# Kernel tuning notes

Measured on AMD Instinct MI355X. Metric: run time of the kernel, lower is better.

Reference implementation:

```python
import jax, jax.numpy as jnp
import numpy as np

NUM_USERS = 50000
NUM_ITEMS = 50000
N_NODES = NUM_USERS + NUM_ITEMS
NNZ = 3200000
EMB_DIM = 64
N_LAYERS = 3
BATCH = 16384


def setup_inputs() -> dict:
    key = jax.random.key(0)
    ks = jax.random.split(key, 7)
    user_emb = 0.1 * jax.random.normal(ks[0], (NUM_USERS, EMB_DIM), dtype=jnp.float32)
    item_emb = 0.1 * jax.random.normal(ks[1], (NUM_ITEMS, EMB_DIM), dtype=jnp.float32)
    edge_val = jax.random.uniform(ks[2], (NNZ,), dtype=jnp.float32)
    edge_src = jax.random.randint(ks[3], (NNZ,), 0, N_NODES, dtype=jnp.int32)
    edge_dst = jax.random.randint(ks[4], (NNZ,), 0, N_NODES, dtype=jnp.int32)
    users = jax.random.randint(ks[5], (BATCH,), 0, NUM_USERS, dtype=jnp.int32)
    items = jax.random.randint(ks[6], (BATCH,), 0, NUM_ITEMS, dtype=jnp.int32)
    return {"user_emb": user_emb, "item_emb": item_emb, "edge_val": edge_val,
            "edge_src": edge_src, "edge_dst": edge_dst, "users": users, "items": items}


def _computer(user_emb, item_emb, edge_val, edge_src, edge_dst):
    # LightGCN propagation: all_emb <- A @ all_emb, mean over layer outputs (incl. layer 0)
    all_emb = jnp.concatenate([user_emb, item_emb], axis=0)  # [N, D]
    acc = all_emb
    for _ in range(N_LAYERS):
        msg = edge_val[:, None] * all_emb[edge_src]          # [nnz, D]
        all_emb = jax.ops.segment_sum(msg, edge_dst, num_segments=N_NODES)
        acc = acc + all_emb
    light_out = acc / jnp.float32(N_LAYERS + 1)
    return light_out[:NUM_USERS], light_out[NUM_USERS:]


def reference(user_emb, item_emb, edge_val, edge_src, edge_dst, users, items):
    all_users, all_items = _computer(user_emb, item_emb, edge_val, edge_src, edge_dst)
    users_emb = all_users[users]                              # [B, D]
    items_emb = all_items[items]                              # [B, D]
    gamma = jnp.sum(users_emb * items_emb, axis=1)            # [B]
    return gamma
```

## Files before the change

kernel.cpp:

```cpp
#include <hip/hip_runtime.h>

#define NUM_USERS 50000
#define NUM_ITEMS 50000
#define N_NODES   100000
#define NNZ       3200000
#define EMB_DIM   64
#define N_LAYERS  3
#define BATCH     16384

#define NBUCK 512
#define ABITS 8
#define NODES_PER_BUCK 256
#define TILE_EDGES 8192
#define NBUCK_USED ((N_NODES + NODES_PER_BUCK - 1) / NODES_PER_BUCK)
#define CAP 9216

typedef unsigned long long ull;
typedef float v2f __attribute__((ext_vector_type(2)));

__device__ inline unsigned bf16pair(float a, float b) {
    unsigned ua = __float_as_uint(a), ub = __float_as_uint(b);
    unsigned r0 = (ua + 0x7fffu + ((ua >> 16) & 1u)) >> 16;
    unsigned r1 = (ub + 0x7fffu + ((ub >> 16) & 1u)) >> 16;
    return r0 | (r1 << 16);
}
__device__ inline float blo(unsigned u) { return __uint_as_float(u << 16); }
__device__ inline float bhi(unsigned u) { return __uint_as_float(u & 0xffff0000u); }

__device__ inline void pkfma(v2f& d, v2f a, v2f b) {
    asm("v_pk_fma_f32 %0, %1, %2, %0" : "+v"(d) : "v"(a), "v"(b));
}
__device__ inline void pkadd(v2f& d, v2f a) {
    asm("v_pk_add_f32 %0, %1, %0" : "+v"(d) : "v"(a));
}

__device__ inline void accP(v2f& sA, v2f& sB, v2f& sC, v2f& sD, uint4 g, unsigned r) {
    float w = (float)(r >> 17);
    v2f w2 = {w, w};
    v2f e0 = {blo(g.x), bhi(g.x)};
    v2f e1 = {blo(g.y), bhi(g.y)};
    v2f e2 = {blo(g.z), bhi(g.z)};
    v2f e3 = {blo(g.w), bhi(g.w)};
    pkfma(sA, e0, w2);
    pkfma(sB, e1, w2);
    pkfma(sC, e2, w2);
    pkfma(sD, e3, w2);
}

__device__ inline uint4 gath(const unsigned char* __restrict__ base, unsigned r, unsigned dOff) {
    unsigned off = ((r & 0x1FFFFu) << 7) + dOff;
    return *(const uint4*)(base + off);
}

__device__ inline uint4 predload4(const unsigned* __restrict__ ep, int j, int b4, int cnt) {
    int i = j + b4;
    uint4 R = *(const uint4*)(ep + i);
    if (i + 1 > cnt) R.x = 0u;
    if (i + 2 > cnt) R.y = 0u;
    if (i + 3 > cnt) R.z = 0u;
    if (i + 4 > cnt) R.w = 0u;
    return R;
}

__device__ inline void wred(v2f& s) {
    v2f t;
    t.x = __shfl_xor(s.x, 8, 64);  t.y = __shfl_xor(s.y, 8, 64);  pkadd(s, t);
    t.x = __shfl_xor(s.x, 16, 64); t.y = __shfl_xor(s.y, 16, 64); pkadd(s, t);
    t.x = __shfl_xor(s.x, 32, 64); t.y = __shfl_xor(s.y, 32, 64); pkadd(s, t);
}

__global__ void init_emb_kernel(const float* __restrict__ ue,
                                const float* __restrict__ ie,
                                unsigned* __restrict__ E0,
                                int* __restrict__ bucketCursor,
                                unsigned char* __restrict__ flags,
                                const int* __restrict__ users,
                                const int* __restrict__ items) {
    int idx = blockIdx.x * blockDim.x + threadIdx.x;
    if (blockIdx.x == 0 && threadIdx.x < 256) {
        bucketCursor[threadIdx.x]       = threadIdx.x * CAP;
        bucketCursor[threadIdx.x + 256] = (threadIdx.x + 256) * CAP;
    }
    if (idx < BATCH) {
        flags[users[idx]] = 1;
    } else if (idx < 2 * BATCH) {
        flags[NUM_USERS + items[idx - BATCH]] = 1;
    }
    const int total = N_NODES * (EMB_DIM / 4);
    if (idx >= total) return;
    const int uoff = NUM_USERS * (EMB_DIM / 4);
    float4 v;
    if (idx < uoff) v = ((const float4*)ue)[idx];
    else            v = ((const float4*)ie)[idx - uoff];
    uint2 h;
    h.x = bf16pair(v.x, v.y);
    h.y = bf16pair(v.z, v.w);
    ((uint2*)E0)[idx] = h;
}

__global__ void partA_kernel(const float* __restrict__ ev,
                             const int*  __restrict__ es,
                             const int*  __restrict__ ed,
                             int* __restrict__ bucketCursor,
                             ull* __restrict__ tmp) {
    __shared__ int hist[NBUCK];
    __shared__ int base[NBUCK];
    __shared__ int cnt2[NBUCK];
    int tid = threadIdx.x;
    int e0 = blockIdx.x * TILE_EDGES;

    int      mySrc[8], myDst[8];
    unsigned myQ[8];

    for (int i = tid; i < NBUCK; i += 1024) hist[i] = 0;
    __syncthreads();

    #pragma unroll
    for (int k = 0; k < 8; ++k) {
        int e = e0 + k * 1024 + tid;
        if (e < NNZ) {
            mySrc[k] = es[e];
            myDst[k] = ed[e];
            myQ[k]   = (unsigned)fminf(ev[e] * 32768.f + 0.5f, 32767.f);
            atomicAdd(&hist[((unsigned)myDst[k]) >> ABITS], 1);
        } else {
            myDst[k] = -1;
        }
    }
    __syncthreads();

    for (int i = tid; i < NBUCK; i += 1024) {
        int c = hist[i];
        base[i] = c ? atomicAdd(&bucketCursor[i], c) : 0;
        cnt2[i] = 0;
    }
    __syncthreads();

    #pragma unroll
    for (int k = 0; k < 8; ++k) {
        int dst = myDst[k];
        if (dst < 0) continue;
        int b = ((unsigned)dst) >> ABITS;
        int pos = base[b] + atomicAdd(&cnt2[b], 1);
        if (pos < (b + 1) * CAP) {
            ull rec = (ull)(unsigned)(mySrc[k] | ((dst & (NODES_PER_BUCK - 1)) << 17))
                    | ((ull)myQ[k] << 25);
            tmp[pos] = rec;
        }
    }
}

__global__ void partB_kernel(const ull* __restrict__ tmp,
                             const int* __restrict__ bucketCursor,
                             int* __restrict__ rowStart,
                             int* __restrict__ deg,
                             unsigned* __restrict__ sorted) {
    __shared__ int cnt[NODES_PER_BUCK];
    __shared__ int sc[NODES_PER_BUCK];
    __shared__ int cur[NODES_PER_BUCK];
    int b = blockIdx.x;
    int tid = threadIdx.x;
    int nodeLo = b << ABITS;
    int startE = b * CAP;
    int endE   = bucketCursor[b];

    if (tid < NODES_PER_BUCK) cnt[tid] = 0;
    __syncthreads();

    ull myRec[9];
    int nRec = 0;
    #pragma unroll
    for (int k = 0; k < 9; ++k) {
        int i = startE + k * 1024 + tid;
        if (i < endE) {
            myRec[k] = tmp[i];
            nRec = k + 1;
            atomicAdd(&cnt[(int)((myRec[k] >> 17) & (NODES_PER_BUCK - 1))], 1);
        }
    }
    __syncthreads();

    if (tid < NODES_PER_BUCK) sc[tid] = (cnt[tid] + 3) & ~3;
    __syncthreads();
    for (int o = 1; o < NODES_PER_BUCK; o <<= 1) {
        int add = 0;
        if (tid < NODES_PER_BUCK && tid >= o) add = sc[tid - o];
        __syncthreads();
        if (tid < NODES_PER_BUCK) sc[tid] += add;
        __syncthreads();
    }
    if (tid < NODES_PER_BUCK) {
        int node = nodeLo + tid;
        int pc = (cnt[tid] + 3) & ~3;
        int rs = startE + sc[tid] - pc;
        cur[tid] = rs;
        if (node < N_NODES) {
            rowStart[node] = rs;
            deg[node] = cnt[tid];
        }
    }
    __syncthreads();

    for (int k = 0; k < nRec; ++k) {
        ull rec = myRec[k];
        int dl = (int)((rec >> 17) & (NODES_PER_BUCK - 1));
        unsigned o = (unsigned)(rec & 0x1FFFFULL) | ((unsigned)((rec >> 25) & 0x7FFF) << 17);
        int pos = atomicAdd(&cur[dl], 1);
        if (pos < startE + CAP) sorted[pos] = o;
    }
}

__global__ void __launch_bounds__(256, 4)
pull_kernel(const unsigned char* __restrict__ A16,
            uint4* __restrict__ B16,
            const unsigned* __restrict__ sorted,
            const int* __restrict__ rowStart,
            const int* __restrict__ deg,
            const unsigned char* __restrict__ flags,
            int gate) {
    int wid = __builtin_amdgcn_readfirstlane((blockIdx.x << 2) + (threadIdx.x >> 6));
    int n0 = wid << 1;
    if (n0 >= N_NODES) return;
    int lane = threadIdx.x & 63;
    int eg = lane >> 3;
    int b4 = eg << 2;
    unsigned dOff = (unsigned)(lane & 7) << 4;

    bool a0 = true, a1 = true;
    if (gate) {
        a0 = flags[n0] == 1;
        a1 = flags[n0 + 1] == 1;
        if (!(a0 || a1)) return;
    }
    int c0 = a0 ? deg[n0] : 0;
    int c1 = a1 ? deg[n0 + 1] : 0;
    const unsigned* ep0 = sorted + rowStart[n0];
    const unsigned* ep1 = sorted + rowStart[n0 + 1];

    bool u0a = c0 > 0,  u0b = c0 > 32;
    bool u1a = c1 > 0,  u1b = c1 > 32;

    uint4 R0a, R1a, R0b, R1b;
    if (u0a) R0a = predload4(ep0, 0,  b4, c0);
    if (u1a) R1a = predload4(ep1, 0,  b4, c1);
    if (u0b) R0b = predload4(ep0, 32, b4, c0);
    if (u1b) R1b = predload4(ep1, 32, b4, c1);

    v2f s0A = {0.f,0.f}, s0B = {0.f,0.f}, s0C = {0.f,0.f}, s0D = {0.f,0.f};
    v2f s1A = {0.f,0.f}, s1B = {0.f,0.f}, s1C = {0.f,0.f}, s1D = {0.f,0.f};

    uint4 G0a0, G0a1, G0a2, G0a3;
    uint4 G1a0, G1a1, G1a2, G1a3;
    uint4 G0b0, G0b1, G0b2, G0b3;
    uint4 G1b0, G1b1, G1b2, G1b3;
    if (u0a) {
        G0a0 = gath(A16, R0a.x, dOff); G0a1 = gath(A16, R0a.y, dOff);
        G0a2 = gath(A16, R0a.z, dOff); G0a3 = gath(A16, R0a.w, dOff);
    }
    if (u1a) {
        G1a0 = gath(A16, R1a.x, dOff); G1a1 = gath(A16, R1a.y, dOff);
        G1a2 = gath(A16, R1a.z, dOff); G1a3 = gath(A16, R1a.w, dOff);
    }
    if (u0b) {
        G0b0 = gath(A16, R0b.x, dOff); G0b1 = gath(A16, R0b.y, dOff);
        G0b2 = gath(A16, R0b.z, dOff); G0b3 = gath(A16, R0b.w, dOff);
    }

    if (u0a) {
        accP(s0A, s0B, s0C, s0D, G0a0, R0a.x);
        accP(s0A, s0B, s0C, s0D, G0a1, R0a.y);
        accP(s0A, s0B, s0C, s0D, G0a2, R0a.z);
        accP(s0A, s0B, s0C, s0D, G0a3, R0a.w);
    }
    if (u1b) {
        G1b0 = gath(A16, R1b.x, dOff); G1b1 = gath(A16, R1b.y, dOff);
        G1b2 = gath(A16, R1b.z, dOff); G1b3 = gath(A16, R1b.w, dOff);
    }
    if (u0b) {
        accP(s0A, s0B, s0C, s0D, G0b0, R0b.x);
        accP(s0A, s0B, s0C, s0D, G0b1, R0b.y);
        accP(s0A, s0B, s0C, s0D, G0b2, R0b.z);
        accP(s0A, s0B, s0C, s0D, G0b3, R0b.w);
    }
    if (u1a) {
        accP(s1A, s1B, s1C, s1D, G1a0, R1a.x);
        accP(s1A, s1B, s1C, s1D, G1a1, R1a.y);
        accP(s1A, s1B, s1C, s1D, G1a2, R1a.z);
        accP(s1A, s1B, s1C, s1D, G1a3, R1a.w);
    }
    if (u1b) {
        accP(s1A, s1B, s1C, s1D, G1b0, R1b.x);
        accP(s1A, s1B, s1C, s1D, G1b1, R1b.y);
        accP(s1A, s1B, s1C, s1D, G1b2, R1b.z);
        accP(s1A, s1B, s1C, s1D, G1b3, R1b.w);
    }

    if (__builtin_expect((c0 > 64) || (c1 > 64), 0)) {
        for (int j = 64; j < c0; j += 16) {
            int i0 = j + eg, i1 = j + 8 + eg;
            unsigned r0 = (i0 < c0) ? ep0[i0] : 0u;
            unsigned r1 = (i1 < c0) ? ep0[i1] : 0u;
            uint4 g0 = gath(A16, r0, dOff);
            uint4 g1 = gath(A16, r1, dOff);
            accP(s0A, s0B, s0C, s0D, g0, r0);
            accP(s0A, s0B, s0C, s0D, g1, r1);
        }
        for (int j = 64; j < c1; j += 16) {
            int i0 = j + eg, i1 = j + 8 + eg;
            unsigned r0 = (i0 < c1) ? ep1[i0] : 0u;
            unsigned r1 = (i1 < c1) ? ep1[i1] : 0u;
            uint4 g0 = gath(A16, r0, dOff);
            uint4 g1 = gath(A16, r1, dOff);
            accP(s1A, s1B, s1C, s1D, g0, r0);
            accP(s1A, s1B, s1C, s1D, g1, r1);
        }
    }

    wred(s0A); wred(s1A); wred(s0B); wred(s1B);
    wred(s0C); wred(s1C); wred(s0D); wred(s1D);

    if (eg == 0) {
        const float k15 = 1.f / 32768.f;
        if (a0) {
            uint4 h;
            h.x = bf16pair(s0A.x * k15, s0A.y * k15);
            h.y = bf16pair(s0B.x * k15, s0B.y * k15);
            h.z = bf16pair(s0C.x * k15, s0C.y * k15);
            h.w = bf16pair(s0D.x * k15, s0D.y * k15);
            B16[(((long long)n0) << 3) + (lane & 7)] = h;
        }
        if (a1) {
            uint4 h;
            h.x = bf16pair(s1A.x * k15, s1A.y * k15);
            h.y = bf16pair(s1B.x * k15, s1B.y * k15);
            h.z = bf16pair(s1C.x * k15, s1C.y * k15);
            h.w = bf16pair(s1D.x * k15, s1D.y * k15);
            B16[(((long long)(n0 + 1)) << 3) + (lane & 7)] = h;
        }
    }
}

__global__ void dot_kernel(const unsigned* __restrict__ E0,
                           const unsigned* __restrict__ B1,
                           const unsigned* __restrict__ B2,
                           const unsigned* __restrict__ B3,
                           const int* __restrict__ users,
                           const int* __restrict__ items,
                           float* __restrict__ out) {
    int t = blockIdx.x * blockDim.x + threadIdx.x;
    int b = t >> 5;
    int lane = t & 31;
    if (b >= BATCH) return;
    long long uo = ((long long)users[b] << 5) + lane;
    long long io = ((long long)(items[b] + NUM_USERS) << 5) + lane;
    unsigned a0 = E0[uo], a1 = B1[uo], a2 = B2[uo], a3 = B3[uo];
    unsigned c0 = E0[io], c1 = B1[io], c2 = B2[io], c3 = B3[io];
    float ux = (blo(a0) + blo(a1)) + (blo(a2) + blo(a3));
    float uy = (bhi(a0) + bhi(a1)) + (bhi(a2) + bhi(a3));
    float ix = (blo(c0) + blo(c1)) + (blo(c2) + blo(c3));
    float iy = (bhi(c0) + bhi(c1)) + (bhi(c2) + bhi(c3));
    float p = ux * ix + uy * iy;
    #pragma unroll
    for (int off = 16; off >= 1; off >>= 1)
        p += __shfl_xor(p, off, 64);
    if (lane == 0) out[b] = p * 0.0625f;
}

extern "C" void kernel_launch(void* const* d_in, const int* in_sizes, int n_in,
                              void* d_out, int out_size, void* d_ws, size_t ws_size,
                              hipStream_t stream) {
    const float* user_emb = (const float*)d_in[0];
    const float* item_emb = (const float*)d_in[1];
    const float* edge_val = (const float*)d_in[2];
    const int*   edge_src = (const int*)d_in[3];
    const int*   edge_dst = (const int*)d_in[4];
    const int*   users    = (const int*)d_in[5];
    const int*   items    = (const int*)d_in[6];
    float* out = (float*)d_out;

    const size_t emb16Bytes = (size_t)N_NODES * EMB_DIM * 2;
    const size_t sortBytes  = (size_t)NBUCK_USED * CAP * sizeof(unsigned);
    const size_t tmpBytes   = (size_t)NBUCK_USED * CAP * sizeof(ull);
    const size_t nodeBytes  = (size_t)N_NODES * sizeof(int);

    char* w = (char*)d_ws;
    unsigned* E0           = (unsigned*)(w); w += emb16Bytes;
    unsigned* B1           = (unsigned*)(w); w += emb16Bytes;
    unsigned* B2           = (unsigned*)(w); w += emb16Bytes;
    unsigned* B3           = (unsigned*)(w); w += emb16Bytes;
    unsigned* sorted       = (unsigned*)(w); w += sortBytes;
    ull*      tmp          = (ull*)(w);      w += tmpBytes;
    int*      deg          = (int*)(w);      w += nodeBytes;
    int*      rowStart     = (int*)(w);      w += nodeBytes;
    int*      bucketCursor = (int*)(w);      w += NBUCK * sizeof(int);
    unsigned char* flags   = (unsigned char*)(w); w += N_NODES;

    const int vecTotal   = N_NODES * (EMB_DIM / 4);
    const int initBlocks = (vecTotal + 255) / 256;
    const int tileBlocks = (NNZ + TILE_EDGES - 1) / TILE_EDGES;

    init_emb_kernel<<<initBlocks, 256, 0, stream>>>(user_emb, item_emb, E0,
                                                    bucketCursor, flags, users, items);

    partA_kernel<<<tileBlocks, 1024, 0, stream>>>(edge_val, edge_src, edge_dst,
                                                  bucketCursor, tmp);
    partB_kernel<<<NBUCK_USED, 1024, 0, stream>>>(tmp, bucketCursor,
                                                  rowStart, deg, sorted);

    const int pullBlocks = ((N_NODES / 2) * 64 + 255) / 256;
    pull_kernel<<<pullBlocks, 256, 0, stream>>>((const unsigned char*)E0, (uint4*)B1,
                                                sorted, rowStart, deg, flags, 0);
    pull_kernel<<<pullBlocks, 256, 0, stream>>>((const unsigned char*)B1, (uint4*)B2,
                                                sorted, rowStart, deg, flags, 0);
    pull_kernel<<<pullBlocks, 256, 0, stream>>>((const unsigned char*)B2, (uint4*)B3,
                                                sorted, rowStart, deg, flags, 1);

    const int dotBlocks = (BATCH * 32 + 255) / 256;
    dot_kernel<<<dotBlocks, 256, 0, stream>>>(E0, B1, B2, B3, users, items, out);
}
```

Measured before the change: 279.7 us.

## Sub-sort edges by source quarter and add per-group SpMM pull kernel

The bucket sort now splits each destination's edge list into four cells by source-node range, recording per-cell degrees in a packed word and zero-padding each cell to a multiple of four. A new pull kernel for the two full layers assigns each 8-lane group its own pair of destination nodes and sweeps the four source ranges in order, so concurrent waves gather from a narrower slice of the embedding table at a time for better cache locality. The last, gated layer keeps the previous kernel. In exchange the sort uses more shared memory and padding, CAP grows, and the 8-bit per-cell degree packing assumes small degrees.

```diff
diff --git a/kernel.cpp b/kernel.cpp
--- a/kernel.cpp
+++ b/kernel.cpp
@@ -13,7 +13,8 @@
 #define NODES_PER_BUCK 256
 #define TILE_EDGES 8192
 #define NBUCK_USED ((N_NODES + NODES_PER_BUCK - 1) / NODES_PER_BUCK)
-#define CAP 9216
+#define CAP 10240
+#define NCELL 1024
 
 typedef unsigned long long ull;
 typedef float v2f __attribute__((ext_vector_type(2)));
@@ -52,6 +53,36 @@
     return *(const uint4*)(base + off);
 }
 
+__device__ inline uint4 pl4(const unsigned* __restrict__ p, int base, int cnt) {
+    uint4 R = *(const uint4*)(p + base);
+    if (base + 1 > cnt) R.x = 0u;
+    if (base + 2 > cnt) R.y = 0u;
+    if (base + 3 > cnt) R.z = 0u;
+    if (base + 4 > cnt) R.w = 0u;
+    return R;
+}
+
+__device__ inline void round4(const unsigned char* __restrict__ A16,
+                              const unsigned* __restrict__ p, int base, int cnt,
+                              unsigned dOff, v2f& sA, v2f& sB, v2f& sC, v2f& sD) {
+    uint4 R = pl4(p, base, cnt);
+    uint4 g0 = gath(A16, R.x, dOff);
+    uint4 g1 = gath(A16, R.y, dOff);
+    uint4 g2 = gath(A16, R.z, dOff);
+    uint4 g3 = gath(A16, R.w, dOff);
+    accP(sA, sB, sC, sD, g0, R.x);
+    accP(sA, sB, sC, sD, g1, R.y);
+    accP(sA, sB, sC, sD, g2, R.z);
+    accP(sA, sB, sC, sD, g3, R.w);
+}
+
+__device__ inline void wred(v2f& s) {
+    v2f t;
+    t.x = __shfl_xor(s.x, 8, 64);  t.y = __shfl_xor(s.y, 8, 64);  pkadd(s, t);
+    t.x = __shfl_xor(s.x, 16, 64); t.y = __shfl_xor(s.y, 16, 64); pkadd(s, t);
+    t.x = __shfl_xor(s.x, 32, 64); t.y = __shfl_xor(s.y, 32, 64); pkadd(s, t);
+}
+
 __device__ inline uint4 predload4(const unsigned* __restrict__ ep, int j, int b4, int cnt) {
     int i = j + b4;
     uint4 R = *(const uint4*)(ep + i);
@@ -60,13 +91,6 @@
     if (i + 3 > cnt) R.z = 0u;
     if (i + 4 > cnt) R.w = 0u;
     return R;
-}
-
-__device__ inline void wred(v2f& s) {
-    v2f t;
-    t.x = __shfl_xor(s.x, 8, 64);  t.y = __shfl_xor(s.y, 8, 64);  pkadd(s, t);
-    t.x = __shfl_xor(s.x, 16, 64); t.y = __shfl_xor(s.y, 16, 64); pkadd(s, t);
-    t.x = __shfl_xor(s.x, 32, 64); t.y = __shfl_xor(s.y, 32, 64); pkadd(s, t);
 }
 
 __global__ void init_emb_kernel(const float* __restrict__ ue,
@@ -154,20 +178,22 @@
                              const int* __restrict__ bucketCursor,
                              int* __restrict__ rowStart,
                              int* __restrict__ deg,
+                             unsigned* __restrict__ degPack,
                              unsigned* __restrict__ sorted) {
-    __shared__ int cnt[NODES_PER_BUCK];
-    __shared__ int sc[NODES_PER_BUCK];
-    __shared__ int cur[NODES_PER_BUCK];
+    __shared__ int cnt[NCELL];
+    __shared__ int sc[NCELL];
+    __shared__ int cur[NCELL];
     int b = blockIdx.x;
     int tid = threadIdx.x;
     int nodeLo = b << ABITS;
     int startE = b * CAP;
     int endE   = bucketCursor[b];
 
-    if (tid < NODES_PER_BUCK) cnt[tid] = 0;
+    cnt[tid] = 0;
     __syncthreads();
 
     ull myRec[9];
+    int myCell[9];
     int nRec = 0;
     #pragma unroll
     for (int k = 0; k < 9; ++k) {
@@ -175,49 +201,119 @@
         if (i < endE) {
             myRec[k] = tmp[i];
             nRec = k + 1;
-            atomicAdd(&cnt[(int)((myRec[k] >> 17) & (NODES_PER_BUCK - 1))], 1);
-        }
-    }
-    __syncthreads();
-
-    if (tid < NODES_PER_BUCK) sc[tid] = (cnt[tid] + 3) & ~3;
-    __syncthreads();
-    for (int o = 1; o < NODES_PER_BUCK; o <<= 1) {
-        int add = 0;
-        if (tid < NODES_PER_BUCK && tid >= o) add = sc[tid - o];
+            unsigned src = (unsigned)(myRec[k] & 0x1FFFFULL);
+            int q = (int)(src >> 15); if (q > 3) q = 3;
+            int dl = (int)((myRec[k] >> 17) & (NODES_PER_BUCK - 1));
+            myCell[k] = (dl << 2) + q;
+            atomicAdd(&cnt[myCell[k]], 1);
+        }
+    }
+    __syncthreads();
+
+    int p4 = (cnt[tid] + 3) & ~3;
+    sc[tid] = p4;
+    __syncthreads();
+    for (int o = 1; o < NCELL; o <<= 1) {
+        int add = (tid >= o) ? sc[tid - o] : 0;
         __syncthreads();
-        if (tid < NODES_PER_BUCK) sc[tid] += add;
+        sc[tid] += add;
         __syncthreads();
     }
+    cur[tid] = startE + sc[tid] - p4;
+    __syncthreads();
+
     if (tid < NODES_PER_BUCK) {
         int node = nodeLo + tid;
-        int pc = (cnt[tid] + 3) & ~3;
-        int rs = startE + sc[tid] - pc;
-        cur[tid] = rs;
         if (node < N_NODES) {
-            rowStart[node] = rs;
-            deg[node] = cnt[tid];
+            int c0 = cnt[tid*4], c1 = cnt[tid*4+1], c2 = cnt[tid*4+2], c3 = cnt[tid*4+3];
+            rowStart[node] = cur[tid*4];
+            deg[node] = sc[tid*4+3] - (sc[tid*4] - ((c0 + 3) & ~3));
+            degPack[node] = (unsigned)c0 | ((unsigned)c1 << 8)
+                          | ((unsigned)c2 << 16) | ((unsigned)c3 << 24);
         }
     }
     __syncthreads();
 
     for (int k = 0; k < nRec; ++k) {
         ull rec = myRec[k];
-        int dl = (int)((rec >> 17) & (NODES_PER_BUCK - 1));
         unsigned o = (unsigned)(rec & 0x1FFFFULL) | ((unsigned)((rec >> 25) & 0x7FFF) << 17);
-        int pos = atomicAdd(&cur[dl], 1);
+        int pos = atomicAdd(&cur[myCell[k]], 1);
         if (pos < startE + CAP) sorted[pos] = o;
     }
+    __syncthreads();
+
+    int cellEnd = startE + sc[tid];
+    for (int p = cur[tid]; p < cellEnd; ++p)
+        if (p < startE + CAP) sorted[p] = 0;
+}
+
+__global__ void __launch_bounds__(256, 6)
+pull_sync_kernel(const unsigned char* __restrict__ A16,
+                 uint4* __restrict__ B16,
+                 const unsigned* __restrict__ sorted,
+                 const int* __restrict__ rowStart,
+                 const unsigned* __restrict__ degPack) {
+    int wid = (blockIdx.x << 2) + (threadIdx.x >> 6);
+    if (wid >= N_NODES / 16) return;
+    int lane = threadIdx.x & 63;
+    int eg = lane >> 3;
+    int d8 = lane & 7;
+    unsigned dOff = (unsigned)d8 << 4;
+    int n0 = (wid << 4) + (eg << 1);
+
+    int off0 = rowStart[n0];
+    int off1 = rowStart[n0 + 1];
+    unsigned dp0 = degPack[n0], dp1 = degPack[n0 + 1];
+
+    v2f s00 = {0.f,0.f}, s01 = {0.f,0.f}, s02 = {0.f,0.f}, s03 = {0.f,0.f};
+    v2f s10 = {0.f,0.f}, s11 = {0.f,0.f}, s12 = {0.f,0.f}, s13 = {0.f,0.f};
+
+    #pragma unroll 1
+    for (int q = 0; q < 4; ++q) {
+        int d0 = (int)(dp0 & 255u); dp0 >>= 8;
+        int d1 = (int)(dp1 & 255u); dp1 >>= 8;
+        const unsigned* p0 = sorted + off0;
+        const unsigned* p1 = sorted + off1;
+        off0 += (d0 + 3) & ~3;
+        off1 += (d1 + 3) & ~3;
+
+        round4(A16, p0, 0, d0, dOff, s00, s01, s02, s03);
+        round4(A16, p1, 0, d1, dOff, s10, s11, s12, s13);
+        round4(A16, p0, 4, d0, dOff, s00, s01, s02, s03);
+        round4(A16, p1, 4, d1, dOff, s10, s11, s12, s13);
+        if (d0 > 8)  round4(A16, p0, 8,  d0, dOff, s00, s01, s02, s03);
+        if (d1 > 8)  round4(A16, p1, 8,  d1, dOff, s10, s11, s12, s13);
+        if (d0 > 12) round4(A16, p0, 12, d0, dOff, s00, s01, s02, s03);
+        if (d1 > 12) round4(A16, p1, 12, d1, dOff, s10, s11, s12, s13);
+        if (__builtin_expect((d0 > 16) || (d1 > 16), 0)) {
+            for (int j = 16; j < d0; j += 4)
+                round4(A16, p0, j, d0, dOff, s00, s01, s02, s03);
+            for (int j = 16; j < d1; j += 4)
+                round4(A16, p1, j, d1, dOff, s10, s11, s12, s13);
+        }
+    }
+
+    const float k15 = 1.f / 32768.f;
+    uint4 h;
+    h.x = bf16pair(s00.x * k15, s00.y * k15);
+    h.y = bf16pair(s01.x * k15, s01.y * k15);
+    h.z = bf16pair(s02.x * k15, s02.y * k15);
+    h.w = bf16pair(s03.x * k15, s03.y * k15);
+    B16[(((long long)n0) << 3) + d8] = h;
+    h.x = bf16pair(s10.x * k15, s10.y * k15);
+    h.y = bf16pair(s11.x * k15, s11.y * k15);
+    h.z = bf16pair(s12.x * k15, s12.y * k15);
+    h.w = bf16pair(s13.x * k15, s13.y * k15);
+    B16[(((long long)(n0 + 1)) << 3) + d8] = h;
 }
 
 __global__ void __launch_bounds__(256, 4)
-pull_kernel(const unsigned char* __restrict__ A16,
-            uint4* __restrict__ B16,
-            const unsigned* __restrict__ sorted,
-            const int* __restrict__ rowStart,
-            const int* __restrict__ deg,
-            const unsigned char* __restrict__ flags,
-            int gate) {
+pull_gated_kernel(const unsigned char* __restrict__ A16,
+                  uint4* __restrict__ B16,
+                  const unsigned* __restrict__ sorted,
+                  const int* __restrict__ rowStart,
+                  const int* __restrict__ deg,
+                  const unsigned char* __restrict__ flags) {
     int wid = __builtin_amdgcn_readfirstlane((blockIdx.x << 2) + (threadIdx.x >> 6));
     int n0 = wid << 1;
     if (n0 >= N_NODES) return;
@@ -226,12 +322,9 @@
     int b4 = eg << 2;
     unsigned dOff = (unsigned)(lane & 7) << 4;
 
-    bool a0 = true, a1 = true;
-    if (gate) {
-        a0 = flags[n0] == 1;
-        a1 = flags[n0 + 1] == 1;
-        if (!(a0 || a1)) return;
-    }
+    bool a0 = flags[n0] == 1;
+    bool a1 = flags[n0 + 1] == 1;
+    if (!(a0 || a1)) return;
     int c0 = a0 ? deg[n0] : 0;
     int c1 = a1 ? deg[n0 + 1] : 0;
     const unsigned* ep0 = sorted + rowStart[n0];
@@ -265,7 +358,6 @@
         G0b0 = gath(A16, R0b.x, dOff); G0b1 = gath(A16, R0b.y, dOff);
         G0b2 = gath(A16, R0b.z, dOff); G0b3 = gath(A16, R0b.w, dOff);
     }
-
     if (u0a) {
         accP(s0A, s0B, s0C, s0D, G0a0, R0a.x);
         accP(s0A, s0B, s0C, s0D, G0a1, R0a.y);
@@ -392,6 +484,7 @@
     ull*      tmp          = (ull*)(w);      w += tmpBytes;
     int*      deg          = (int*)(w);      w += nodeBytes;
     int*      rowStart     = (int*)(w);      w += nodeBytes;
+    unsigned* degPack      = (unsigned*)(w); w += nodeBytes;
     int*      bucketCursor = (int*)(w);      w += NBUCK * sizeof(int);
     unsigned char* flags   = (unsigned char*)(w); w += N_NODES;
 
@@ -405,15 +498,18 @@
     partA_kernel<<<tileBlocks, 1024, 0, stream>>>(edge_val, edge_src, edge_dst,
                                                   bucketCursor, tmp);
     partB_kernel<<<NBUCK_USED, 1024, 0, stream>>>(tmp, bucketCursor,
-                                                  rowStart, deg, sorted);
-
-    const int pullBlocks = ((N_NODES / 2) * 64 + 255) / 256;
-    pull_kernel<<<pullBlocks, 256, 0, stream>>>((const unsigned char*)E0, (uint4*)B1,
-                                                sorted, rowStart, deg, flags, 0);
-    pull_kernel<<<pullBlocks, 256, 0, stream>>>((const unsigned char*)B1, (uint4*)B2,
-                                                sorted, rowStart, deg, flags, 0);
-    pull_kernel<<<pullBlocks, 256, 0, stream>>>((const unsigned char*)B2, (uint4*)B3,
-                                                sorted, rowStart, deg, flags, 1);
+                                                  rowStart, deg, degPack, sorted);
+
+    const int syncWaves  = N_NODES / 16;
+    const int syncBlocks = (syncWaves + 3) / 4;
+    pull_sync_kernel<<<syncBlocks, 256, 0, stream>>>((const unsigned char*)E0, (uint4*)B1,
+                                                     sorted, rowStart, degPack);
+    pull_sync_kernel<<<syncBlocks, 256, 0, stream>>>((const unsigned char*)B1, (uint4*)B2,
+                                                     sorted, rowStart, degPack);
+
+    const int gatedBlocks = ((N_NODES / 2) * 64 + 255) / 256;
+    pull_gated_kernel<<<gatedBlocks, 256, 0, stream>>>((const unsigned char*)B2, (uint4*)B3,
+                                                       sorted, rowStart, deg, flags);
 
     const int dotBlocks = (BATCH * 32 + 255) / 256;
     dot_kernel<<<dotBlocks, 256, 0, stream>>>(E0, B1, B2, B3, users, items, out);
```

Result: no change. 284.3 us (+1.7%).
